# Optimization experiments

Measured on AMD Instinct MI355X. Metric: run time of the kernel, lower is better.

Reference implementation:

```python
import jax, jax.numpy as jnp
import numpy as np

B, T, D, H = 2, 2048, 1024, 16
DH = D // H

def setup_inputs() -> dict:
    key = jax.random.key(0)
    ks = jax.random.split(key, 6)
    s = 0.02
    return {
        "x": jax.random.normal(ks[0], (B, T, D), jnp.float32),
        "Wq": jax.random.normal(ks[1], (D, D), jnp.float32) * s,
        "Wk": jax.random.normal(ks[2], (D, D), jnp.float32) * s,
        "Wv": jax.random.normal(ks[3], (D, D), jnp.float32) * s,
        "Wo": jax.random.normal(ks[4], (D, D), jnp.float32) * s,
        "bo": jnp.zeros((D,), jnp.float32),
    }

def reference(x, Wq, Wk, Wv, Wo, bo):
    Bx, Tx, _ = x.shape
    # project and split heads: [B, H, T, DH]
    q = (x @ Wq).reshape(Bx, Tx, H, DH).transpose(0, 2, 1, 3)
    k = (x @ Wk).reshape(Bx, Tx, H, DH).transpose(0, 2, 1, 3)
    v = (x @ Wv).reshape(Bx, Tx, H, DH).transpose(0, 2, 1, 3)
    scores = jnp.einsum("bhqd,bhkd->bhqk", q, k)  # [B,H,T,T]
    causal = jnp.triu(jnp.ones((Tx, Tx), bool), k=1)  # True above diagonal
    scores = jnp.where(causal, -jnp.inf, scores)
    # original scales AFTER masking (equivalent math)
    w = jax.nn.softmax(scores / jnp.sqrt(jnp.float32(DH)), axis=-1)
    # dropout p=0.0 -> identity
    ctx = jnp.einsum("bhqk,bhkd->bhqd", w, v)
    ctx = ctx.transpose(0, 2, 1, 3).reshape(Bx, Tx, D)
    return ctx @ Wo + bo
```

## Files before the change

kernel.cpp:

```cpp
#include <hip/hip_runtime.h>
#include <hip/hip_bf16.h>


typedef __bf16 bf16x8 __attribute__((ext_vector_type(8)));
typedef __bf16 bf16x4 __attribute__((ext_vector_type(4)));
typedef float  f32x4  __attribute__((ext_vector_type(4)));

#define Bx 2
#define Tx 2048
#define Dx 1024
#define Hx 16
#define DHx 64

__global__ __launch_bounds__(256) void cvt_x(const float* __restrict__ x, __bf16* __restrict__ xb) {
    int i = (blockIdx.x * 256 + threadIdx.x) * 4;
    float4 v = *(const float4*)(x + i);
    bf16x4 o;
    o[0] = (__bf16)v.x; o[1] = (__bf16)v.y; o[2] = (__bf16)v.z; o[3] = (__bf16)v.w;
    *(bf16x4*)(xb + i) = o;
}

__global__ __launch_bounds__(256) void transpose_cvt(const float* __restrict__ W0,
                                                     const float* __restrict__ W1,
                                                     const float* __restrict__ W2,
                                                     const float* __restrict__ W3,
                                                     __bf16* __restrict__ out) {
    __shared__ float tile[64][65];
    int z = blockIdx.z;
    const float* W = (z == 0) ? W0 : (z == 1) ? W1 : (z == 2) ? W2 : W3;
    __bf16* o = out + (size_t)z * Dx * Dx;
    int k0 = blockIdx.x * 64, n0 = blockIdx.y * 64;
    int t = threadIdx.x;
    int cc = t & 63, rbase = t >> 6;
#pragma unroll
    for (int i = 0; i < 16; i++) {
        int rr = rbase + i * 4;
        tile[rr][cc] = W[(size_t)(k0 + rr) * Dx + n0 + cc];
    }
    __syncthreads();
#pragma unroll
    for (int i = 0; i < 16; i++) {
        int rr = rbase + i * 4;
        o[(size_t)(n0 + rr) * Dx + k0 + cc] = (__bf16)tile[cc][rr];
    }
}

static __device__ __forceinline__ void gload16(const __bf16* g, __bf16* l) {
    __builtin_amdgcn_global_load_lds((const __attribute__((address_space(1))) void*)g,
                                     (__attribute__((address_space(3))) void*)l, 16, 0, 0);
}

__global__ __launch_bounds__(256) void gemm_qkv(const __bf16* __restrict__ A,
                                                const __bf16* __restrict__ BT,
                                                __bf16* __restrict__ Qb,
                                                __bf16* __restrict__ Kb,
                                                __bf16* __restrict__ Vt) {
    __shared__ __bf16 As[128 * 32];
    __shared__ __bf16 Bs[128 * 32];
    const int t = threadIdx.x;
    const int lane = t & 63, wave = t >> 6;
    const int lane15 = lane & 15, quad = lane >> 4;
    const int m0 = blockIdx.x * 128, n0 = blockIdx.y * 128;
    const int wm = wave & 1, wn = wave >> 1;

    const int sr = wave * 32 + (lane >> 2), sc = (lane & 3) * 8;
    const __bf16* Ag = A + (size_t)(m0 + sr) * Dx + sc;
    const __bf16* Bg = BT + (size_t)(n0 + sr) * Dx + sc;
    __bf16* Asl0 = As + (wave * 32) * 32;
    __bf16* Asl1 = As + (wave * 32 + 16) * 32;
    __bf16* Bsl0 = Bs + (wave * 32) * 32;
    __bf16* Bsl1 = Bs + (wave * 32 + 16) * 32;

    f32x4 acc[4][4];
#pragma unroll
    for (int i = 0; i < 4; i++)
#pragma unroll
        for (int j = 0; j < 4; j++) acc[i][j] = (f32x4){0.f, 0.f, 0.f, 0.f};

    for (int k0 = 0; k0 < Dx; k0 += 32) {
        gload16(Ag, Asl0);
        gload16(Ag + 16 * Dx, Asl1);
        gload16(Bg, Bsl0);
        gload16(Bg + 16 * Dx, Bsl1);
        Ag += 32; Bg += 32;
        __syncthreads();
        bf16x8 af[4], bf[4];
#pragma unroll
        for (int i = 0; i < 4; i++) {
            af[i] = *(const bf16x8*)&As[(wm * 64 + i * 16 + lane15) * 32 + quad * 8];
            bf[i] = *(const bf16x8*)&Bs[(wn * 64 + i * 16 + lane15) * 32 + quad * 8];
        }
#pragma unroll
        for (int mt = 0; mt < 4; mt++)
#pragma unroll
            for (int nt = 0; nt < 4; nt++)
                acc[mt][nt] = __builtin_amdgcn_mfma_f32_16x16x32_bf16(af[mt], bf[nt], acc[mt][nt], 0, 0, 0);
        __syncthreads();
    }

    const int z = n0 >> 10;
    if (z < 2) {
        __bf16* outp = z ? Kb : Qb;
        const float scale = z ? 1.0f : 0.125f;
#pragma unroll
        for (int mt = 0; mt < 4; mt++)
#pragma unroll
            for (int nt = 0; nt < 4; nt++) {
                const int cc = (n0 + wn * 64 + nt * 16 + lane15) & 1023;
                const int h = cc >> 6, dh = cc & 63;
#pragma unroll
                for (int r4 = 0; r4 < 4; r4++) {
                    const int row = m0 + wm * 64 + mt * 16 + quad * 4 + r4;
                    const int b = row >> 11, tt = row & 2047;
                    outp[(((size_t)(b * Hx + h) * Tx + tt) << 6) + dh] =
                        (__bf16)(acc[mt][nt][r4] * scale);
                }
            }
    } else {
#pragma unroll
        for (int mt = 0; mt < 4; mt++)
#pragma unroll
            for (int nt = 0; nt < 4; nt++) {
                const int cc = (n0 + wn * 64 + nt * 16 + lane15) & 1023;
                const int h = cc >> 6, dh = cc & 63;
#pragma unroll
                for (int r4 = 0; r4 < 4; r4++) {
                    const int row = m0 + wm * 64 + mt * 16 + quad * 4 + r4;
                    const int b = row >> 11, tt = row & 2047;
                    Vt[((size_t)(b * Hx + h) * DHx + dh) * Tx + tt] = (__bf16)acc[mt][nt][r4];
                }
            }
    }
}

__global__ __launch_bounds__(256) void gemm_out(const __bf16* __restrict__ A,
                                                const __bf16* __restrict__ BT,
                                                float* __restrict__ outf,
                                                const float* __restrict__ bias) {
    __shared__ __bf16 As[64 * 32];
    __shared__ __bf16 Bs[128 * 32];
    const int t = threadIdx.x;
    const int lane = t & 63, wave = t >> 6;
    const int lane15 = lane & 15, quad = lane >> 4;
    const int m0 = blockIdx.x * 64, n0 = blockIdx.y * 128;

    const int srA = wave * 16 + (lane >> 2), scA = (lane & 3) * 8;
    const int srB = wave * 32 + (lane >> 2);
    const __bf16* Ag = A + (size_t)(m0 + srA) * Dx + scA;
    const __bf16* Bg = BT + (size_t)(n0 + srB) * Dx + scA;
    __bf16* AslA = As + (wave * 16) * 32;
    __bf16* Bsl0 = Bs + (wave * 32) * 32;
    __bf16* Bsl1 = Bs + (wave * 32 + 16) * 32;

    f32x4 acc[4][2];
#pragma unroll
    for (int i = 0; i < 4; i++)
#pragma unroll
        for (int j = 0; j < 2; j++) acc[i][j] = (f32x4){0.f, 0.f, 0.f, 0.f};

    for (int k0 = 0; k0 < Dx; k0 += 32) {
        gload16(Ag, AslA);
        gload16(Bg, Bsl0);
        gload16(Bg + 16 * Dx, Bsl1);
        Ag += 32; Bg += 32;
        __syncthreads();
        bf16x8 af[4], bf[2];
#pragma unroll
        for (int i = 0; i < 4; i++)
            af[i] = *(const bf16x8*)&As[(i * 16 + lane15) * 32 + quad * 8];
#pragma unroll
        for (int i = 0; i < 2; i++)
            bf[i] = *(const bf16x8*)&Bs[(wave * 32 + i * 16 + lane15) * 32 + quad * 8];
#pragma unroll
        for (int mt = 0; mt < 4; mt++)
#pragma unroll
            for (int nt = 0; nt < 2; nt++)
                acc[mt][nt] = __builtin_amdgcn_mfma_f32_16x16x32_bf16(af[mt], bf[nt], acc[mt][nt], 0, 0, 0);
        __syncthreads();
    }

#pragma unroll
    for (int mt = 0; mt < 4; mt++)
#pragma unroll
        for (int nt = 0; nt < 2; nt++) {
            const int col = n0 + wave * 32 + nt * 16 + lane15;
#pragma unroll
            for (int r4 = 0; r4 < 4; r4++) {
                const int row = m0 + mt * 16 + quad * 4 + r4;
                outf[(size_t)row * Dx + col] = acc[mt][nt][r4] + bias[col];
            }
        }
}

__global__ __launch_bounds__(256) void attn_mfma(const __bf16* __restrict__ Q,
                                                 const __bf16* __restrict__ K,
                                                 const __bf16* __restrict__ Vt,
                                                 __bf16* __restrict__ ctx) {
    __shared__ __bf16 Ks[64 * 72];
    __shared__ __bf16 Vs[64 * 72];
    __shared__ __bf16 Ps[64 * 72];
    const int t = threadIdx.x;
    const int lane = t & 63, wave = t >> 6;
    const int lane15 = lane & 15, quad = lane >> 4;
    const int h = blockIdx.y, b = blockIdx.z;
    const size_t headoff = ((size_t)(b * Hx + h)) * Tx * DHx;
    const __bf16* Kbase = K + headoff;
    const __bf16* Vbase = Vt + headoff;
    const int qrow = wave * 16 + quad * 4;
    const int sr = t >> 2, sc = (t & 3) * 16;

    for (int pass = 0; pass < 2; pass++) {
        const int chunk = pass ? (Tx / 64 - 1 - blockIdx.x) : blockIdx.x;
        const int q0 = chunk * 64;

        bf16x8 qf0, qf1;
        {
            const __bf16* Qp = Q + headoff + (size_t)(q0 + wave * 16 + lane15) * 64 + quad * 8;
            qf0 = *(const bf16x8*)Qp;
            qf1 = *(const bf16x8*)(Qp + 32);
        }
        f32x4 o[4];
#pragma unroll
        for (int i = 0; i < 4; i++) o[i] = (f32x4){0.f, 0.f, 0.f, 0.f};
        float lpart[4] = {0.f, 0.f, 0.f, 0.f};

        bf16x8 kpre0, kpre1, vpre0, vpre1;
        {
            const __bf16* Kp = Kbase + (size_t)sr * 64 + sc;
            kpre0 = *(const bf16x8*)Kp; kpre1 = *(const bf16x8*)(Kp + 8);
            const __bf16* Vp = Vbase + (size_t)sr * Tx + sc;
            vpre0 = *(const bf16x8*)Vp; vpre1 = *(const bf16x8*)(Vp + 8);
        }

        for (int kt = 0; kt <= chunk; kt++) {
            __syncthreads();
            *(bf16x8*)&Ks[sr * 72 + sc] = kpre0;
            *(bf16x8*)&Ks[sr * 72 + sc + 8] = kpre1;
            *(bf16x8*)&Vs[sr * 72 + sc] = vpre0;
            *(bf16x8*)&Vs[sr * 72 + sc + 8] = vpre1;
            __syncthreads();
            if (kt < chunk) {
                const __bf16* Kp = Kbase + (size_t)((kt + 1) * 64 + sr) * 64 + sc;
                kpre0 = *(const bf16x8*)Kp; kpre1 = *(const bf16x8*)(Kp + 8);
                const __bf16* Vp = Vbase + (size_t)sr * Tx + (kt + 1) * 64 + sc;
                vpre0 = *(const bf16x8*)Vp; vpre1 = *(const bf16x8*)(Vp + 8);
            }

            f32x4 s[4];
#pragma unroll
            for (int nt = 0; nt < 4; nt++) {
                s[nt] = (f32x4){0.f, 0.f, 0.f, 0.f};
                bf16x8 b0 = *(const bf16x8*)&Ks[(nt * 16 + lane15) * 72 + quad * 8];
                s[nt] = __builtin_amdgcn_mfma_f32_16x16x32_bf16(qf0, b0, s[nt], 0, 0, 0);
                bf16x8 b1 = *(const bf16x8*)&Ks[(nt * 16 + lane15) * 72 + 32 + quad * 8];
                s[nt] = __builtin_amdgcn_mfma_f32_16x16x32_bf16(qf1, b1, s[nt], 0, 0, 0);
            }

            const bool diag = (kt == chunk);
#pragma unroll
            for (int nt = 0; nt < 4; nt++)
#pragma unroll
                for (int reg = 0; reg < 4; reg++) {
                    float e = __expf(s[nt][reg]);
                    if (diag && (nt * 16 + lane15 > qrow + reg)) e = 0.f;
                    lpart[reg] += e;
                    Ps[(qrow + reg) * 72 + nt * 16 + lane15] = (__bf16)e;
                }

            bf16x8 pa0 = *(const bf16x8*)&Ps[(wave * 16 + lane15) * 72 + quad * 8];
            bf16x8 pa1 = *(const bf16x8*)&Ps[(wave * 16 + lane15) * 72 + 32 + quad * 8];
#pragma unroll
            for (int dt = 0; dt < 4; dt++) {
                bf16x8 vb0 = *(const bf16x8*)&Vs[(dt * 16 + lane15) * 72 + quad * 8];
                o[dt] = __builtin_amdgcn_mfma_f32_16x16x32_bf16(pa0, vb0, o[dt], 0, 0, 0);
                bf16x8 vb1 = *(const bf16x8*)&Vs[(dt * 16 + lane15) * 72 + 32 + quad * 8];
                o[dt] = __builtin_amdgcn_mfma_f32_16x16x32_bf16(pa1, vb1, o[dt], 0, 0, 0);
            }
        }

        float inv[4];
#pragma unroll
        for (int reg = 0; reg < 4; reg++) {
            float l = lpart[reg];
#pragma unroll
            for (int off = 1; off < 16; off <<= 1) l += __shfl_xor(l, off);
            inv[reg] = 1.f / l;
        }
#pragma unroll
        for (int dt = 0; dt < 4; dt++)
#pragma unroll
            for (int reg = 0; reg < 4; reg++) {
                int q = q0 + wave * 16 + quad * 4 + reg;
                ctx[(((size_t)(b * Tx + q)) * Hx + h) * 64 + dt * 16 + lane15] =
                    (__bf16)(o[dt][reg] * inv[reg]);
            }
        __syncthreads();
    }
}

extern "C" void kernel_launch(void* const* d_in, const int* in_sizes, int n_in,
                              void* d_out, int out_size, void* d_ws, size_t ws_size,
                              hipStream_t stream) {
    const float* x  = (const float*)d_in[0];
    const float* Wq = (const float*)d_in[1];
    const float* Wk = (const float*)d_in[2];
    const float* Wv = (const float*)d_in[3];
    const float* Wo = (const float*)d_in[4];
    const float* bo = (const float*)d_in[5];
    float* out = (float*)d_out;

    char* ws = (char*)d_ws;
    __bf16* xb  = (__bf16*)(ws + 0);
    __bf16* Wt  = (__bf16*)(ws + (8ull << 20));
    __bf16* Qb  = (__bf16*)(ws + (16ull << 20));
    __bf16* Kb  = (__bf16*)(ws + (24ull << 20));
    __bf16* Vtg = (__bf16*)(ws + (32ull << 20));
    __bf16* ctx = (__bf16*)(ws + (40ull << 20));

    cvt_x<<<dim3((Bx * Tx * Dx) / 1024), 256, 0, stream>>>(x, xb);
    transpose_cvt<<<dim3(16, 16, 4), 256, 0, stream>>>(Wq, Wk, Wv, Wo, Wt);

    gemm_qkv<<<dim3(Bx * Tx / 128, 3 * Dx / 128), 256, 0, stream>>>(xb, Wt, Qb, Kb, Vtg);

    attn_mfma<<<dim3(Tx / 128, Hx, Bx), 256, 0, stream>>>(Qb, Kb, Vtg, ctx);

    gemm_out<<<dim3(Bx * Tx / 64, Dx / 128), 256, 0, stream>>>(ctx, Wt + 3 * (1u << 20), out, bo);
}
```

Before: 192.6 us.

## Enlarge attention query tile to 128 rows and fuse prep conversion kernels

The attention kernel now uses 512 threads (8 waves) per block covering 128 query rows, so each K/V tile loaded into shared memory is reused by twice as many waves. Waves whose rows lie entirely before a key tile skip its compute, and a per-element causal mask replaces the diagonal-only one. The grid is halved, which lowers the number of blocks available to fill the device. Separately, the x conversion and the weight transpose-convert are merged into a single prep launch to save one kernel launch.

```diff
diff --git a/kernel.cpp b/kernel.cpp
--- a/kernel.cpp
+++ b/kernel.cpp
@@ -12,23 +12,30 @@
 #define Hx 16
 #define DHx 64
 
-__global__ __launch_bounds__(256) void cvt_x(const float* __restrict__ x, __bf16* __restrict__ xb) {
-    int i = (blockIdx.x * 256 + threadIdx.x) * 4;
-    float4 v = *(const float4*)(x + i);
-    bf16x4 o;
-    o[0] = (__bf16)v.x; o[1] = (__bf16)v.y; o[2] = (__bf16)v.z; o[3] = (__bf16)v.w;
-    *(bf16x4*)(xb + i) = o;
-}
-
-__global__ __launch_bounds__(256) void transpose_cvt(const float* __restrict__ W0,
-                                                     const float* __restrict__ W1,
-                                                     const float* __restrict__ W2,
-                                                     const float* __restrict__ W3,
-                                                     __bf16* __restrict__ out) {
+__global__ __launch_bounds__(256) void prep(const float* __restrict__ x,
+                                            const float* __restrict__ W0,
+                                            const float* __restrict__ W1,
+                                            const float* __restrict__ W2,
+                                            const float* __restrict__ W3,
+                                            __bf16* __restrict__ xb,
+                                            __bf16* __restrict__ Wt) {
+    const int z = blockIdx.z;
+    if (z == 0) {
+        const int blk = blockIdx.y * 16 + blockIdx.x;
+        const float* xp = x + (size_t)blk * 16384;
+        __bf16* xo = xb + (size_t)blk * 16384;
+#pragma unroll
+        for (int i = 0; i < 16; i++) {
+            float4 v = *(const float4*)(xp + i * 1024 + threadIdx.x * 4);
+            bf16x4 o;
+            o[0] = (__bf16)v.x; o[1] = (__bf16)v.y; o[2] = (__bf16)v.z; o[3] = (__bf16)v.w;
+            *(bf16x4*)(xo + i * 1024 + threadIdx.x * 4) = o;
+        }
+        return;
+    }
     __shared__ float tile[64][65];
-    int z = blockIdx.z;
-    const float* W = (z == 0) ? W0 : (z == 1) ? W1 : (z == 2) ? W2 : W3;
-    __bf16* o = out + (size_t)z * Dx * Dx;
+    const float* W = (z == 1) ? W0 : (z == 2) ? W1 : (z == 3) ? W2 : W3;
+    __bf16* o = Wt + (size_t)(z - 1) * Dx * Dx;
     int k0 = blockIdx.x * 64, n0 = blockIdx.y * 64;
     int t = threadIdx.x;
     int cc = t & 63, rbase = t >> 6;
@@ -192,26 +199,27 @@
         }
 }
 
-__global__ __launch_bounds__(256) void attn_mfma(const __bf16* __restrict__ Q,
+__global__ __launch_bounds__(512) void attn_mfma(const __bf16* __restrict__ Q,
                                                  const __bf16* __restrict__ K,
                                                  const __bf16* __restrict__ Vt,
                                                  __bf16* __restrict__ ctx) {
     __shared__ __bf16 Ks[64 * 72];
     __shared__ __bf16 Vs[64 * 72];
-    __shared__ __bf16 Ps[64 * 72];
+    __shared__ __bf16 Ps[128 * 80];
     const int t = threadIdx.x;
     const int lane = t & 63, wave = t >> 6;
-    const int lane15 = lane & 15, quad = lane >> 4;
+    const int lane15 = lane & 15, quad = (lane >> 4) & 3;
     const int h = blockIdx.y, b = blockIdx.z;
     const size_t headoff = ((size_t)(b * Hx + h)) * Tx * DHx;
     const __bf16* Kbase = K + headoff;
     const __bf16* Vbase = Vt + headoff;
-    const int qrow = wave * 16 + quad * 4;
-    const int sr = t >> 2, sc = (t & 3) * 16;
+    const int sr = t >> 3, sc = (t & 7) * 8;
 
     for (int pass = 0; pass < 2; pass++) {
-        const int chunk = pass ? (Tx / 64 - 1 - blockIdx.x) : blockIdx.x;
-        const int q0 = chunk * 64;
+        const int chunk = pass ? (15 - blockIdx.x) : blockIdx.x;
+        const int q0 = chunk * 128;
+        const int ktiles = 2 * chunk + 2;
+        const int qg = q0 + wave * 16 + quad * 4;
 
         bf16x8 qf0, qf1;
         {
@@ -224,27 +232,19 @@
         for (int i = 0; i < 4; i++) o[i] = (f32x4){0.f, 0.f, 0.f, 0.f};
         float lpart[4] = {0.f, 0.f, 0.f, 0.f};
 
-        bf16x8 kpre0, kpre1, vpre0, vpre1;
-        {
-            const __bf16* Kp = Kbase + (size_t)sr * 64 + sc;
-            kpre0 = *(const bf16x8*)Kp; kpre1 = *(const bf16x8*)(Kp + 8);
-            const __bf16* Vp = Vbase + (size_t)sr * Tx + sc;
-            vpre0 = *(const bf16x8*)Vp; vpre1 = *(const bf16x8*)(Vp + 8);
-        }
-
-        for (int kt = 0; kt <= chunk; kt++) {
+        bf16x8 kpre = *(const bf16x8*)(Kbase + (size_t)sr * 64 + sc);
+        bf16x8 vpre = *(const bf16x8*)(Vbase + (size_t)sr * Tx + sc);
+
+        for (int kt = 0; kt < ktiles; kt++) {
             __syncthreads();
-            *(bf16x8*)&Ks[sr * 72 + sc] = kpre0;
-            *(bf16x8*)&Ks[sr * 72 + sc + 8] = kpre1;
-            *(bf16x8*)&Vs[sr * 72 + sc] = vpre0;
-            *(bf16x8*)&Vs[sr * 72 + sc + 8] = vpre1;
+            *(bf16x8*)&Ks[sr * 72 + sc] = kpre;
+            *(bf16x8*)&Vs[sr * 72 + sc] = vpre;
             __syncthreads();
-            if (kt < chunk) {
-                const __bf16* Kp = Kbase + (size_t)((kt + 1) * 64 + sr) * 64 + sc;
-                kpre0 = *(const bf16x8*)Kp; kpre1 = *(const bf16x8*)(Kp + 8);
-                const __bf16* Vp = Vbase + (size_t)sr * Tx + (kt + 1) * 64 + sc;
-                vpre0 = *(const bf16x8*)Vp; vpre1 = *(const bf16x8*)(Vp + 8);
-            }
+            if (kt + 1 < ktiles) {
+                kpre = *(const bf16x8*)(Kbase + (size_t)((kt + 1) * 64 + sr) * 64 + sc);
+                vpre = *(const bf16x8*)(Vbase + (size_t)sr * Tx + (kt + 1) * 64 + sc);
+            }
+            if (kt * 64 > q0 + wave * 16 + 15) continue;
 
             f32x4 s[4];
 #pragma unroll
@@ -256,19 +256,19 @@
                 s[nt] = __builtin_amdgcn_mfma_f32_16x16x32_bf16(qf1, b1, s[nt], 0, 0, 0);
             }
 
-            const bool diag = (kt == chunk);
+            const int kbase = kt * 64;
 #pragma unroll
             for (int nt = 0; nt < 4; nt++)
 #pragma unroll
                 for (int reg = 0; reg < 4; reg++) {
                     float e = __expf(s[nt][reg]);
-                    if (diag && (nt * 16 + lane15 > qrow + reg)) e = 0.f;
+                    if (kbase + nt * 16 + lane15 > qg + reg) e = 0.f;
                     lpart[reg] += e;
-                    Ps[(qrow + reg) * 72 + nt * 16 + lane15] = (__bf16)e;
+                    Ps[(wave * 16 + quad * 4 + reg) * 80 + nt * 16 + lane15] = (__bf16)e;
                 }
 
-            bf16x8 pa0 = *(const bf16x8*)&Ps[(wave * 16 + lane15) * 72 + quad * 8];
-            bf16x8 pa1 = *(const bf16x8*)&Ps[(wave * 16 + lane15) * 72 + 32 + quad * 8];
+            bf16x8 pa0 = *(const bf16x8*)&Ps[(wave * 16 + lane15) * 80 + quad * 8];
+            bf16x8 pa1 = *(const bf16x8*)&Ps[(wave * 16 + lane15) * 80 + 32 + quad * 8];
 #pragma unroll
             for (int dt = 0; dt < 4; dt++) {
                 bf16x8 vb0 = *(const bf16x8*)&Vs[(dt * 16 + lane15) * 72 + quad * 8];
@@ -294,7 +294,6 @@
                 ctx[(((size_t)(b * Tx + q)) * Hx + h) * 64 + dt * 16 + lane15] =
                     (__bf16)(o[dt][reg] * inv[reg]);
             }
-        __syncthreads();
     }
 }
 
@@ -317,12 +316,11 @@
     __bf16* Vtg = (__bf16*)(ws + (32ull << 20));
     __bf16* ctx = (__bf16*)(ws + (40ull << 20));
 
-    cvt_x<<<dim3((Bx * Tx * Dx) / 1024), 256, 0, stream>>>(x, xb);
-    transpose_cvt<<<dim3(16, 16, 4), 256, 0, stream>>>(Wq, Wk, Wv, Wo, Wt);
+    prep<<<dim3(16, 16, 5), 256, 0, stream>>>(x, Wq, Wk, Wv, Wo, xb, Wt);
 
     gemm_qkv<<<dim3(Bx * Tx / 128, 3 * Dx / 128), 256, 0, stream>>>(xb, Wt, Qb, Kb, Vtg);
 
-    attn_mfma<<<dim3(Tx / 128, Hx, Bx), 256, 0, stream>>>(Qb, Kb, Vtg, ctx);
+    attn_mfma<<<dim3(Tx / 256, Hx, Bx), 512, 0, stream>>>(Qb, Kb, Vtg, ctx);
 
     gemm_out<<<dim3(Bx * Tx / 64, Dx / 128), 256, 0, stream>>>(ctx, Wt + 3 * (1u << 20), out, bo);
 }
```

New measurement: 190.2 us. No clear change (-1.3%).
